# Optimization experiments

Measured on AMD Instinct MI355X. Metric: run time of the kernel, lower is better.

Reference implementation:

```python
import jax, jax.numpy as jnp
import numpy as np

VOCAB, NUM_LABELS, EMB, H = 50000, 5, 512, 1024
B, S = 32, 256


def setup_inputs() -> dict:
    key = jax.random.key(0)
    ks = jax.random.split(key, 7)
    tokens = jax.random.randint(ks[0], (B, S), 0, VOCAB)
    scale_e = 0.05
    emb = jax.random.normal(ks[1], (VOCAB, EMB), dtype=jnp.float32) * scale_e
    # Keras LSTM kernels: input kernel [EMB,4H], recurrent kernel [H,4H], bias [4H]
    W = jax.random.normal(ks[2], (EMB, 4 * H), dtype=jnp.float32) / np.sqrt(EMB)
    U = jax.random.normal(ks[3], (H, 4 * H), dtype=jnp.float32) / np.sqrt(H)
    # unit_forget_bias=True: forget-gate bias block initialized to 1
    b = jnp.concatenate([
        jnp.zeros((H,), jnp.float32),
        jnp.ones((H,), jnp.float32),
        jnp.zeros((2 * H,), jnp.float32),
    ])
    Wd = jax.random.normal(ks[4], (H, NUM_LABELS), dtype=jnp.float32) / np.sqrt(H)
    bd = jnp.zeros((NUM_LABELS,), jnp.float32)
    return {"tokens": tokens, "emb": emb, "W": W, "U": U, "b": b, "Wd": Wd, "bd": bd}


def _lstm_last_h(x, W, U, b):
    # x: [B,S,EMB] -> last hidden state [B,H]
    xt = jnp.swapaxes(x, 0, 1)  # [S,B,EMB]
    # precompute input projections for all steps: [S,B,4H]
    xz = jnp.einsum('sbe,eg->sbg', xt, W) + b
    h0 = jnp.zeros((x.shape[0], H), x.dtype)
    c0 = jnp.zeros((x.shape[0], H), x.dtype)

    def step(carry, xz_t):
        h, c = carry
        z = xz_t + h @ U  # [B,4H]
        i, f, g, o = jnp.split(z, 4, axis=-1)  # Keras gate order i,f,c,o
        i = jax.nn.sigmoid(i)
        f = jax.nn.sigmoid(f)
        g = jnp.tanh(g)
        o = jax.nn.sigmoid(o)
        c = f * c + i * g
        h = o * jnp.tanh(c)
        return (h, c), None

    (h_last, _), _ = jax.lax.scan(step, (h0, c0), xz)
    return h_last


def reference(tokens, emb, W, U, b, Wd, bd):
    x = emb[tokens]  # [B,S,EMB] embedding lookup
    h = _lstm_last_h(x, W, U, b)  # [B,H]
    logits = h @ Wd + bd  # [B,NUM_LABELS]
    return logits
```

## Files before the change

kernel.cpp:

```cpp
#include <hip/hip_runtime.h>
#include <hip/hip_fp16.h>

#define B_   32
#define S_   256
#define EMB_ 512
#define H_   1024
#define G4_  4096
#define NL_  5
#define NBLK 128

typedef short bf16x8 __attribute__((ext_vector_type(8)));
typedef _Float16 f16x8 __attribute__((ext_vector_type(8)));
typedef float f32x4 __attribute__((ext_vector_type(4)));
typedef unsigned long long ull;

__device__ inline unsigned short f2bf(float x) {
  unsigned u = __float_as_uint(x);
  return (unsigned short)((u + 0x7FFF + ((u >> 16) & 1)) >> 16);
}
__device__ inline float bf2f(unsigned short b) {
  return __uint_as_float(((unsigned)b) << 16);
}
__device__ inline ull ldq(const ull* p) {
  return __hip_atomic_load(p, __ATOMIC_RELAXED, __HIP_MEMORY_SCOPE_AGENT);
}
__device__ inline void stw(unsigned* p, unsigned v) {
  __hip_atomic_store(p, v, __ATOMIC_RELAXED, __HIP_MEMORY_SCOPE_AGENT);
}

__global__ __launch_bounds__(256) void k_transposeK(const float* __restrict__ src,
                                                    float* __restrict__ dst, int K) {
  __shared__ float tile[32][33];
  int c0 = blockIdx.x * 32, k0 = blockIdx.y * 32;
  int tx = threadIdx.x & 31, ty = threadIdx.x >> 5;
#pragma unroll
  for (int i = 0; i < 4; ++i)
    tile[ty + 8 * i][tx] = src[(size_t)(k0 + ty + 8 * i) * G4_ + c0 + tx];
  __syncthreads();
#pragma unroll
  for (int i = 0; i < 4; ++i)
    dst[(size_t)(c0 + ty + 8 * i) * K + k0 + tx] = tile[tx][ty + 8 * i];
}

__global__ __launch_bounds__(256) void k_prep(const float* __restrict__ Ut,
                                              bf16x8* __restrict__ Ubf) {
  int gid = blockIdx.x * 256 + threadIdx.x;
  int l = gid & 63;
  int bxws = gid >> 6;
  int n = l & 15, kgrp = l >> 4;
  int s = bxws & 7, bw = bxws >> 3;
  int w = bw & 3, bx = bw >> 2;
  int g = n & 3, ju = n >> 2;
  int gcol = g * 1024 + bx * 4 + ju;
  int kbase = w * 256 + s * 32 + kgrp * 8;
  const float4* f = (const float4*)(Ut + (size_t)gcol * H_ + kbase);
  float4 f0 = f[0], f1 = f[1];
  float v[8] = {f0.x, f0.y, f0.z, f0.w, f1.x, f1.y, f1.z, f1.w};
  bf16x8 vh, vl;
#pragma unroll
  for (int j = 0; j < 8; ++j) {
    unsigned short hi = f2bf(v[j]);
    vh[j] = (short)hi;
    vl[j] = (short)f2bf(v[j] - bf2f(hi));
  }
  Ubf[(size_t)bxws * 128 + l] = vh;
  Ubf[(size_t)bxws * 128 + 64 + l] = vl;
}

__global__ __launch_bounds__(256) void k_prepW16(const float* __restrict__ Wt,
                                                 unsigned short* __restrict__ Wf16) {
  int gid = blockIdx.x * 256 + threadIdx.x;
  int l = gid & 63, fi = gid >> 6;
  int kc = fi & 15, ug = fi >> 4;
  int n16 = l & 15, kgrp = l >> 4;
  int gcol = (n16 & 3) * 1024 + ug * 4 + (n16 >> 2);
  const float4* f = (const float4*)(Wt + (size_t)gcol * 512 + kc * 32 + kgrp * 8);
  float4 f0 = f[0], f1 = f[1];
  float v[8] = {f0.x, f0.y, f0.z, f0.w, f1.x, f1.y, f1.z, f1.w};
  union { unsigned short u[8]; uint4 q; } o;
#pragma unroll
  for (int j = 0; j < 8; ++j) o.u[j] = __half_as_ushort(__float2half_rn(v[j]));
  *(uint4*)(Wf16 + ((size_t)fi * 64 + l) * 8) = o.q;
}

__global__ __launch_bounds__(256) void k_prepX(const int* __restrict__ tokens,
                                               const float* __restrict__ emb,
                                               unsigned short* __restrict__ Xf16) {
  int gid = blockIdx.x * 256 + threadIdx.x;
  int seg = gid & 63, row = gid >> 6;
  int s = row >> 5, b = row & 31;
  int tok = tokens[b * 256 + s];
  const float4* f = (const float4*)(emb + (size_t)tok * EMB_ + seg * 8);
  float4 f0 = f[0], f1 = f[1];
  float v[8] = {f0.x, f0.y, f0.z, f0.w, f1.x, f1.y, f1.z, f1.w};
  union { unsigned short u[8]; uint4 q; } o;
#pragma unroll
  for (int j = 0; j < 8; ++j) o.u[j] = __half_as_ushort(__float2half_rn(v[j]));
  *(uint4*)(Xf16 + (size_t)row * 512 + seg * 8) = o.q;
}

__global__ __launch_bounds__(512, 2) void k_steps6(
    const bf16x8* __restrict__ Ubf,
    const unsigned short* __restrict__ Wf16,
    const unsigned short* __restrict__ Xf16,
    const float* __restrict__ bias,
    unsigned* __restrict__ Hh0, unsigned* __restrict__ Hl0,
    unsigned* __restrict__ Hh1, unsigned* __restrict__ Hl1,
    unsigned* __restrict__ flg) {
  __shared__ bf16x8 UL[8192];
  __shared__ float red[4096];
  __shared__ float zg[1056];
  __shared__ float bias_s[32];

  const int tid = threadIdx.x;
  const int bx = blockIdx.x;
  const int l = tid & 63, w = tid >> 6;

#pragma unroll
  for (int i = 0; i < 16; ++i) {
    int flat = i * 512 + tid;
    int ll = flat & 63, s8 = (flat >> 6) & 7, ks = (flat >> 9) & 3;
    int pl = (flat >> 11) & 1, cg = flat >> 12;
    size_t fi = (size_t)((bx * 2 + cg) * 4 + ks) * 8 + s8;
    UL[flat] = Ubf[fi * 128 + pl * 64 + ll];
  }
  if (tid < 32) {
    int cg = tid >> 4, n16 = tid & 15;
    bias_s[tid] = bias[(n16 & 3) * 1024 + (bx * 2 + cg) * 4 + (n16 >> 2)];
  }

  const int e = tid & 255, m = tid >> 8;
  const int n16r = (e >> 2) & 15;
  const int zb = m * 16 + (e >> 6) * 4 + (e & 3);

  const int gb = tid & 31, gu = tid >> 5;
  const int gk = bx * 8 + gu;
  const int widx = (gb >> 4) * 8192 + (gk >> 3) * 64 + (gb & 15) * 4 + ((gk & 7) >> 1);
  const int zrd = gb * 33 + (gu >> 2) * 16 + (gu & 3) * 4;
  float creg = 0.f;

  const int ks_w = w >> 1;
  const unsigned* myflg = flg + (w * 16 + (l & 15)) * 32;

  const int xrow0 = (l & 15) * 512 + (l >> 4) * 8;

  __syncthreads();

  for (int t = 0; t < S_; ++t) {
    const ull* RdH = (const ull*)((t & 1) ? Hh0 : Hh1);
    const ull* RdL = (const ull*)((t & 1) ? Hl0 : Hl1);
    unsigned* WrH = (t & 1) ? Hh1 : Hh0;
    unsigned* WrL = (t & 1) ? Hl1 : Hl0;

    f32x4 acc[2][2];
#pragma unroll
    for (int cg = 0; cg < 2; ++cg) {
      acc[cg][0] = (f32x4){0.f, 0.f, 0.f, 0.f};
      acc[cg][1] = (f32x4){0.f, 0.f, 0.f, 0.f};
    }
    {
      const unsigned short* Xt = Xf16 + (size_t)t * 16384;
#pragma unroll
      for (int c2 = 0; c2 < 2; ++c2) {
        int kc = w * 2 + c2;
        f16x8 xa0 = *(const f16x8*)(Xt + xrow0 + kc * 32);
        f16x8 xa1 = *(const f16x8*)(Xt + 8192 + xrow0 + kc * 32);
        f16x8 wb0 = *(const f16x8*)(Wf16 + ((size_t)((bx * 2 + 0) * 16 + kc) * 64 + l) * 8);
        f16x8 wb1 = *(const f16x8*)(Wf16 + ((size_t)((bx * 2 + 1) * 16 + kc) * 64 + l) * 8);
        acc[0][0] = __builtin_amdgcn_mfma_f32_16x16x32_f16(xa0, wb0, acc[0][0], 0, 0, 0);
        acc[0][1] = __builtin_amdgcn_mfma_f32_16x16x32_f16(xa1, wb0, acc[0][1], 0, 0, 0);
        acc[1][0] = __builtin_amdgcn_mfma_f32_16x16x32_f16(xa0, wb1, acc[1][0], 0, 0, 0);
        acc[1][1] = __builtin_amdgcn_mfma_f32_16x16x32_f16(xa1, wb1, acc[1][1], 0, 0, 0);
      }
    }

    if (t > 0) {
      while (true) {
        unsigned v = __hip_atomic_load(myflg, __ATOMIC_RELAXED, __HIP_MEMORY_SCOPE_AGENT);
        if (__all((int)(v >= (unsigned)t))) break;
        __builtin_amdgcn_s_sleep(1);
      }
      union F { ull q[2]; bf16x8 v; };
      F A[4][4];
#pragma unroll
      for (int s = 0; s < 4; ++s) {
        int i0 = (w * 16 + s * 4) * 32 + l * 2;
        A[s][0].q[0] = ldq(RdH + i0);        A[s][0].q[1] = ldq(RdH + i0 + 1);
        A[s][1].q[0] = ldq(RdH + 4096 + i0); A[s][1].q[1] = ldq(RdH + 4096 + i0 + 1);
        A[s][2].q[0] = ldq(RdL + i0);        A[s][2].q[1] = ldq(RdL + i0 + 1);
        A[s][3].q[0] = ldq(RdL + 4096 + i0); A[s][3].q[1] = ldq(RdL + 4096 + i0 + 1);
      }
#pragma unroll
      for (int s = 0; s < 4; ++s) {
        int s8 = (w & 1) * 4 + s;
#pragma unroll
        for (int cg = 0; cg < 2; ++cg) {
          bf16x8 uhf = UL[((cg * 2 + 0) * 4 + ks_w) * 512 + s8 * 64 + l];
          bf16x8 ulf = UL[((cg * 2 + 1) * 4 + ks_w) * 512 + s8 * 64 + l];
          acc[cg][0] = __builtin_amdgcn_mfma_f32_16x16x32_bf16(A[s][0].v, uhf, acc[cg][0], 0, 0, 0);
          acc[cg][1] = __builtin_amdgcn_mfma_f32_16x16x32_bf16(A[s][1].v, uhf, acc[cg][1], 0, 0, 0);
          acc[cg][0] = __builtin_amdgcn_mfma_f32_16x16x32_bf16(A[s][2].v, uhf, acc[cg][0], 0, 0, 0);
          acc[cg][1] = __builtin_amdgcn_mfma_f32_16x16x32_bf16(A[s][3].v, uhf, acc[cg][1], 0, 0, 0);
          acc[cg][0] = __builtin_amdgcn_mfma_f32_16x16x32_bf16(A[s][0].v, ulf, acc[cg][0], 0, 0, 0);
          acc[cg][1] = __builtin_amdgcn_mfma_f32_16x16x32_bf16(A[s][1].v, ulf, acc[cg][1], 0, 0, 0);
        }
      }
    }

    if (w < 4) {
#pragma unroll
      for (int cg = 0; cg < 2; ++cg) {
        *(f32x4*)(&red[((w * 2 + 0) * 2 + cg) * 256 + l * 4]) = acc[cg][0];
        *(f32x4*)(&red[((w * 2 + 1) * 2 + cg) * 256 + l * 4]) = acc[cg][1];
      }
    }
    __syncthreads();
    if (w >= 4) {
      int w4 = w - 4;
#pragma unroll
      for (int cg = 0; cg < 2; ++cg) {
        f32x4* p0 = (f32x4*)(&red[((w4 * 2 + 0) * 2 + cg) * 256 + l * 4]);
        f32x4* p1 = (f32x4*)(&red[((w4 * 2 + 1) * 2 + cg) * 256 + l * 4]);
        *p0 += acc[cg][0];
        *p1 += acc[cg][1];
      }
    }
    __syncthreads();

    {
      float z0 = bias_s[n16r], z1 = bias_s[16 + n16r];
#pragma unroll
      for (int w4 = 0; w4 < 4; ++w4) {
        z0 += red[((w4 * 2 + m) * 2 + 0) * 256 + e];
        z1 += red[((w4 * 2 + m) * 2 + 1) * 256 + e];
      }
      zg[zb * 33 + n16r] = z0;
      zg[zb * 33 + 16 + n16r] = z1;
    }
    __syncthreads();

    if (tid < 256) {
      float zi = zg[zrd + 0];
      float zf = zg[zrd + 1];
      float zc_ = zg[zrd + 2];
      float zo = zg[zrd + 3];
      float ig = 1.f / (1.f + __expf(-zi));
      float fg = 1.f / (1.f + __expf(-zf));
      float gg = tanhf(zc_);
      float og = 1.f / (1.f + __expf(-zo));
      creg = fg * creg + ig * gg;
      float hv = og * tanhf(creg);
      unsigned short hh_ = f2bf(hv);
      unsigned short hl_ = f2bf(hv - bf2f(hh_));
      unsigned pk = (unsigned)hh_ | ((unsigned)hl_ << 16);
      unsigned other = (unsigned)__shfl_xor((int)pk, 32, 64);
      if ((gu & 1) == 0)
        stw(WrH + widx, (pk & 0xffffu) | (other << 16));
      else
        stw(WrL + widx, (other >> 16) | (pk & 0xffff0000u));
    }
    __syncthreads();
    if (tid == 0)
      stw(flg + bx * 32, (unsigned)(t + 1));
  }
}

__global__ __launch_bounds__(256) void k_head4(const unsigned* __restrict__ Hh,
                                               const unsigned* __restrict__ Hl,
                                               const float* __restrict__ Wd,
                                               const float* __restrict__ bd,
                                               float* __restrict__ out) {
  __shared__ float red[32 * 9];
  int lbl = blockIdx.x;
  int tid = threadIdx.x;
  int b = tid >> 3, ks = tid & 7;
  int mb = (b >> 4) * 8192 + (b & 15) * 4;
  float acc = 0.f;
  for (int k = ks * 128; k < ks * 128 + 128; ++k) {
    int idx = mb + (k >> 3) * 64 + ((k & 7) >> 1);
    int sh = (k & 1) * 16;
    float hv = bf2f((unsigned short)((Hh[idx] >> sh) & 0xffffu)) +
               bf2f((unsigned short)((Hl[idx] >> sh) & 0xffffu));
    acc += hv * Wd[k * NL_ + lbl];
  }
  red[b * 9 + ks] = acc;
  __syncthreads();
  if (tid < 32) {
    float s = bd[lbl];
#pragma unroll
    for (int i = 0; i < 8; ++i) s += red[tid * 9 + i];
    out[tid * NL_ + lbl] = s;
  }
}

extern "C" void kernel_launch(void* const* d_in, const int* in_sizes, int n_in,
                              void* d_out, int out_size, void* d_ws, size_t ws_size,
                              hipStream_t stream) {
  const int* tokens  = (const int*)d_in[0];
  const float* emb   = (const float*)d_in[1];
  const float* W     = (const float*)d_in[2];
  const float* U     = (const float*)d_in[3];
  const float* bias  = (const float*)d_in[4];
  const float* Wd    = (const float*)d_in[5];
  const float* bd    = (const float*)d_in[6];
  float* out = (float*)d_out;

  char* ws = (char*)d_ws;
  unsigned short* Xf16 = (unsigned short*)ws;
  unsigned short* Wf16 = (unsigned short*)(ws + 8388608);
  float* Ut          = (float*)(ws + 16777216);
  float* Wt          = (float*)(ws + 33554432);
  bf16x8* Ubf        = (bf16x8*)(ws + 67108864);
  unsigned* Hh0      = (unsigned*)(ws + 83886080);
  unsigned* Hl0      = (unsigned*)(ws + 83886080 + 65536);
  unsigned* Hh1      = (unsigned*)(ws + 83886080 + 131072);
  unsigned* Hl1      = (unsigned*)(ws + 83886080 + 196608);
  unsigned* flg      = (unsigned*)(ws + 84148224);

  hipMemsetAsync(flg, 0, 16384, stream);
  k_transposeK<<<dim3(128, 32), 256, 0, stream>>>(U, Ut, 1024);
  k_prep<<<2048, 256, 0, stream>>>(Ut, Ubf);
  k_transposeK<<<dim3(128, 16), 256, 0, stream>>>(W, Wt, 512);
  k_prepW16<<<1024, 256, 0, stream>>>(Wt, Wf16);
  k_prepX<<<2048, 256, 0, stream>>>(tokens, emb, Xf16);

  k_steps6<<<NBLK, 512, 0, stream>>>(Ubf, Wf16, Xf16, bias,
                                     Hh0, Hl0, Hh1, Hl1, flg);

  k_head4<<<NL_, 256, 0, stream>>>(Hh1, Hl1, Wd, bd, out);
}
```

Baseline: 1.190 ms.

## Tag hidden-state words with step number and drop per-block flag barrier

Replaces the per-step flag counter and its trailing __syncthreads with step-tagged hidden-state words: each 32-bit store packs the fp16 h value with the step index, and readers spin on the data itself until every tag matches. The hidden state drops from a bf16 hi/lo pair to a single fp16 value, and U is split into an fp16 hi part plus a residual scaled by 1024. This cuts the recurrent MFMA count and removes one global round trip per step. In exchange, h is carried at fp16 precision, and the 16-bit step tag limits the pattern to short sequences.

```diff
diff --git a/kernel.cpp b/kernel.cpp
--- a/kernel.cpp
+++ b/kernel.cpp
@@ -9,18 +9,10 @@
 #define NL_  5
 #define NBLK 128
 
-typedef short bf16x8 __attribute__((ext_vector_type(8)));
 typedef _Float16 f16x8 __attribute__((ext_vector_type(8)));
 typedef float f32x4 __attribute__((ext_vector_type(4)));
 typedef unsigned long long ull;
 
-__device__ inline unsigned short f2bf(float x) {
-  unsigned u = __float_as_uint(x);
-  return (unsigned short)((u + 0x7FFF + ((u >> 16) & 1)) >> 16);
-}
-__device__ inline float bf2f(unsigned short b) {
-  return __uint_as_float(((unsigned)b) << 16);
-}
 __device__ inline ull ldq(const ull* p) {
   return __hip_atomic_load(p, __ATOMIC_RELAXED, __HIP_MEMORY_SCOPE_AGENT);
 }
@@ -42,8 +34,8 @@
     dst[(size_t)(c0 + ty + 8 * i) * K + k0 + tx] = tile[tx][ty + 8 * i];
 }
 
-__global__ __launch_bounds__(256) void k_prep(const float* __restrict__ Ut,
-                                              bf16x8* __restrict__ Ubf) {
+__global__ __launch_bounds__(256) void k_prepU16(const float* __restrict__ Ut,
+                                                 f16x8* __restrict__ Ubf) {
   int gid = blockIdx.x * 256 + threadIdx.x;
   int l = gid & 63;
   int bxws = gid >> 6;
@@ -56,12 +48,12 @@
   const float4* f = (const float4*)(Ut + (size_t)gcol * H_ + kbase);
   float4 f0 = f[0], f1 = f[1];
   float v[8] = {f0.x, f0.y, f0.z, f0.w, f1.x, f1.y, f1.z, f1.w};
-  bf16x8 vh, vl;
+  f16x8 vh, vl;
 #pragma unroll
   for (int j = 0; j < 8; ++j) {
-    unsigned short hi = f2bf(v[j]);
-    vh[j] = (short)hi;
-    vl[j] = (short)f2bf(v[j] - bf2f(hi));
+    _Float16 hi = (_Float16)v[j];
+    vh[j] = hi;
+    vl[j] = (_Float16)((v[j] - (float)hi) * 1024.f);
   }
   Ubf[(size_t)bxws * 128 + l] = vh;
   Ubf[(size_t)bxws * 128 + 64 + l] = vl;
@@ -99,15 +91,13 @@
   *(uint4*)(Xf16 + (size_t)row * 512 + seg * 8) = o.q;
 }
 
-__global__ __launch_bounds__(512, 2) void k_steps6(
-    const bf16x8* __restrict__ Ubf,
+__global__ __launch_bounds__(512, 2) void k_steps7(
+    const f16x8* __restrict__ Ubf,
     const unsigned short* __restrict__ Wf16,
     const unsigned short* __restrict__ Xf16,
     const float* __restrict__ bias,
-    unsigned* __restrict__ Hh0, unsigned* __restrict__ Hl0,
-    unsigned* __restrict__ Hh1, unsigned* __restrict__ Hl1,
-    unsigned* __restrict__ flg) {
-  __shared__ bf16x8 UL[8192];
+    unsigned* __restrict__ T0, unsigned* __restrict__ T1) {
+  __shared__ f16x8 UL[8192];
   __shared__ float red[4096];
   __shared__ float zg[1056];
   __shared__ float bias_s[32];
@@ -134,29 +124,27 @@
   const int zb = m * 16 + (e >> 6) * 4 + (e & 3);
 
   const int gb = tid & 31, gu = tid >> 5;
-  const int gk = bx * 8 + gu;
-  const int widx = (gb >> 4) * 8192 + (gk >> 3) * 64 + (gb & 15) * 4 + ((gk & 7) >> 1);
+  const int widx = (gb >> 4) * 16384 + (bx >> 2) * 512 +
+                   ((bx & 3) * 16 + (gb & 15)) * 8 + gu;
   const int zrd = gb * 33 + (gu >> 2) * 16 + (gu & 3) * 4;
   float creg = 0.f;
 
   const int ks_w = w >> 1;
-  const unsigned* myflg = flg + (w * 16 + (l & 15)) * 32;
-
   const int xrow0 = (l & 15) * 512 + (l >> 4) * 8;
 
   __syncthreads();
 
   for (int t = 0; t < S_; ++t) {
-    const ull* RdH = (const ull*)((t & 1) ? Hh0 : Hh1);
-    const ull* RdL = (const ull*)((t & 1) ? Hl0 : Hl1);
-    unsigned* WrH = (t & 1) ? Hh1 : Hh0;
-    unsigned* WrL = (t & 1) ? Hl1 : Hl0;
-
-    f32x4 acc[2][2];
+    const ull* R64 = (const ull*)((t & 1) ? T0 : T1);
+    unsigned* WrT = (t & 1) ? T1 : T0;
+
+    f32x4 acc[2][2], accL[2][2];
 #pragma unroll
     for (int cg = 0; cg < 2; ++cg) {
       acc[cg][0] = (f32x4){0.f, 0.f, 0.f, 0.f};
       acc[cg][1] = (f32x4){0.f, 0.f, 0.f, 0.f};
+      accL[cg][0] = (f32x4){0.f, 0.f, 0.f, 0.f};
+      accL[cg][1] = (f32x4){0.f, 0.f, 0.f, 0.f};
     }
     {
       const unsigned short* Xt = Xf16 + (size_t)t * 16384;
@@ -175,36 +163,59 @@
     }
 
     if (t > 0) {
-      while (true) {
-        unsigned v = __hip_atomic_load(myflg, __ATOMIC_RELAXED, __HIP_MEMORY_SCOPE_AGENT);
-        if (__all((int)(v >= (unsigned)t))) break;
-        __builtin_amdgcn_s_sleep(1);
-      }
-      union F { ull q[2]; bf16x8 v; };
-      F A[4][4];
-#pragma unroll
-      for (int s = 0; s < 4; ++s) {
-        int i0 = (w * 16 + s * 4) * 32 + l * 2;
-        A[s][0].q[0] = ldq(RdH + i0);        A[s][0].q[1] = ldq(RdH + i0 + 1);
-        A[s][1].q[0] = ldq(RdH + 4096 + i0); A[s][1].q[1] = ldq(RdH + 4096 + i0 + 1);
-        A[s][2].q[0] = ldq(RdL + i0);        A[s][2].q[1] = ldq(RdL + i0 + 1);
-        A[s][3].q[0] = ldq(RdL + 4096 + i0); A[s][3].q[1] = ldq(RdL + 4096 + i0 + 1);
-      }
+      ull A[2][4][4];
+      const unsigned tg = (unsigned)(t - 1);
+      bool ok;
+      do {
+#pragma unroll
+        for (int m2 = 0; m2 < 2; ++m2)
+#pragma unroll
+          for (int s = 0; s < 4; ++s) {
+            int ib = m2 * 8192 + (w * 4 + s) * 256 + l * 4;
+#pragma unroll
+            for (int i = 0; i < 4; ++i) A[m2][s][i] = ldq(R64 + ib + i);
+          }
+        unsigned bad = 0;
+#pragma unroll
+        for (int m2 = 0; m2 < 2; ++m2)
+#pragma unroll
+          for (int s = 0; s < 4; ++s)
+#pragma unroll
+            for (int i = 0; i < 4; ++i) {
+              ull q = A[m2][s][i];
+              bad |= (((unsigned)(q >> 16)) & 0xffffu) ^ tg;
+              bad |= ((unsigned)(q >> 48)) ^ tg;
+            }
+        ok = __all(bad == 0);
+        if (!ok) __builtin_amdgcn_s_sleep(1);
+      } while (!ok);
+
 #pragma unroll
       for (int s = 0; s < 4; ++s) {
         int s8 = (w & 1) * 4 + s;
+        union { unsigned u[4]; f16x8 v; } a0, a1;
+#pragma unroll
+        for (int i = 0; i < 4; ++i) {
+          ull q0 = A[0][s][i], q1 = A[1][s][i];
+          a0.u[i] = ((unsigned)q0 & 0xffffu) | (((unsigned)(q0 >> 16)) & 0xffff0000u);
+          a1.u[i] = ((unsigned)q1 & 0xffffu) | (((unsigned)(q1 >> 16)) & 0xffff0000u);
+        }
 #pragma unroll
         for (int cg = 0; cg < 2; ++cg) {
-          bf16x8 uhf = UL[((cg * 2 + 0) * 4 + ks_w) * 512 + s8 * 64 + l];
-          bf16x8 ulf = UL[((cg * 2 + 1) * 4 + ks_w) * 512 + s8 * 64 + l];
-          acc[cg][0] = __builtin_amdgcn_mfma_f32_16x16x32_bf16(A[s][0].v, uhf, acc[cg][0], 0, 0, 0);
-          acc[cg][1] = __builtin_amdgcn_mfma_f32_16x16x32_bf16(A[s][1].v, uhf, acc[cg][1], 0, 0, 0);
-          acc[cg][0] = __builtin_amdgcn_mfma_f32_16x16x32_bf16(A[s][2].v, uhf, acc[cg][0], 0, 0, 0);
-          acc[cg][1] = __builtin_amdgcn_mfma_f32_16x16x32_bf16(A[s][3].v, uhf, acc[cg][1], 0, 0, 0);
-          acc[cg][0] = __builtin_amdgcn_mfma_f32_16x16x32_bf16(A[s][0].v, ulf, acc[cg][0], 0, 0, 0);
-          acc[cg][1] = __builtin_amdgcn_mfma_f32_16x16x32_bf16(A[s][1].v, ulf, acc[cg][1], 0, 0, 0);
+          f16x8 uhf = UL[cg * 4096 + ks_w * 512 + s8 * 64 + l];
+          f16x8 ulf = UL[cg * 4096 + 2048 + ks_w * 512 + s8 * 64 + l];
+          acc[cg][0]  = __builtin_amdgcn_mfma_f32_16x16x32_f16(a0.v, uhf, acc[cg][0], 0, 0, 0);
+          acc[cg][1]  = __builtin_amdgcn_mfma_f32_16x16x32_f16(a1.v, uhf, acc[cg][1], 0, 0, 0);
+          accL[cg][0] = __builtin_amdgcn_mfma_f32_16x16x32_f16(a0.v, ulf, accL[cg][0], 0, 0, 0);
+          accL[cg][1] = __builtin_amdgcn_mfma_f32_16x16x32_f16(a1.v, ulf, accL[cg][1], 0, 0, 0);
         }
       }
+    }
+
+#pragma unroll
+    for (int cg = 0; cg < 2; ++cg) {
+      acc[cg][0] += accL[cg][0] * 9.765625e-4f;
+      acc[cg][1] += accL[cg][1] * 9.765625e-4f;
     }
 
     if (w < 4) {
@@ -250,23 +261,13 @@
       float og = 1.f / (1.f + __expf(-zo));
       creg = fg * creg + ig * gg;
       float hv = og * tanhf(creg);
-      unsigned short hh_ = f2bf(hv);
-      unsigned short hl_ = f2bf(hv - bf2f(hh_));
-      unsigned pk = (unsigned)hh_ | ((unsigned)hl_ << 16);
-      unsigned other = (unsigned)__shfl_xor((int)pk, 32, 64);
-      if ((gu & 1) == 0)
-        stw(WrH + widx, (pk & 0xffffu) | (other << 16));
-      else
-        stw(WrL + widx, (other >> 16) | (pk & 0xffff0000u));
-    }
-    __syncthreads();
-    if (tid == 0)
-      stw(flg + bx * 32, (unsigned)(t + 1));
-  }
-}
-
-__global__ __launch_bounds__(256) void k_head4(const unsigned* __restrict__ Hh,
-                                               const unsigned* __restrict__ Hl,
+      unsigned short h16 = __half_as_ushort(__float2half_rn(hv));
+      stw(WrT + widx, ((unsigned)t << 16) | (unsigned)h16);
+    }
+  }
+}
+
+__global__ __launch_bounds__(256) void k_head5(const unsigned* __restrict__ T,
                                                const float* __restrict__ Wd,
                                                const float* __restrict__ bd,
                                                float* __restrict__ out) {
@@ -274,13 +275,11 @@
   int lbl = blockIdx.x;
   int tid = threadIdx.x;
   int b = tid >> 3, ks = tid & 7;
-  int mb = (b >> 4) * 8192 + (b & 15) * 4;
+  int mb = (b >> 4) * 16384;
   float acc = 0.f;
   for (int k = ks * 128; k < ks * 128 + 128; ++k) {
-    int idx = mb + (k >> 3) * 64 + ((k & 7) >> 1);
-    int sh = (k & 1) * 16;
-    float hv = bf2f((unsigned short)((Hh[idx] >> sh) & 0xffffu)) +
-               bf2f((unsigned short)((Hl[idx] >> sh) & 0xffffu));
+    int idx = mb + (k >> 5) * 512 + (((k >> 3) & 3) * 16 + (b & 15)) * 8 + (k & 7);
+    float hv = __half2float(__ushort_as_half((unsigned short)(T[idx] & 0xffffu)));
     acc += hv * Wd[k * NL_ + lbl];
   }
   red[b * 9 + ks] = acc;
@@ -310,22 +309,18 @@
   unsigned short* Wf16 = (unsigned short*)(ws + 8388608);
   float* Ut          = (float*)(ws + 16777216);
   float* Wt          = (float*)(ws + 33554432);
-  bf16x8* Ubf        = (bf16x8*)(ws + 67108864);
-  unsigned* Hh0      = (unsigned*)(ws + 83886080);
-  unsigned* Hl0      = (unsigned*)(ws + 83886080 + 65536);
-  unsigned* Hh1      = (unsigned*)(ws + 83886080 + 131072);
-  unsigned* Hl1      = (unsigned*)(ws + 83886080 + 196608);
-  unsigned* flg      = (unsigned*)(ws + 84148224);
-
-  hipMemsetAsync(flg, 0, 16384, stream);
+  f16x8* Ubf         = (f16x8*)(ws + 67108864);
+  unsigned* T0       = (unsigned*)(ws + 83886080);
+  unsigned* T1       = (unsigned*)(ws + 83886080 + 131072);
+
+  hipMemsetAsync(T0, 0xFF, 262144, stream);
   k_transposeK<<<dim3(128, 32), 256, 0, stream>>>(U, Ut, 1024);
-  k_prep<<<2048, 256, 0, stream>>>(Ut, Ubf);
+  k_prepU16<<<2048, 256, 0, stream>>>(Ut, Ubf);
   k_transposeK<<<dim3(128, 16), 256, 0, stream>>>(W, Wt, 512);
   k_prepW16<<<1024, 256, 0, stream>>>(Wt, Wf16);
   k_prepX<<<2048, 256, 0, stream>>>(tokens, emb, Xf16);
 
-  k_steps6<<<NBLK, 512, 0, stream>>>(Ubf, Wf16, Xf16, bias,
-                                     Hh0, Hl0, Hh1, Hl1, flg);
-
-  k_head4<<<NL_, 256, 0, stream>>>(Hh1, Hl1, Wd, bd, out);
-}
+  k_steps7<<<NBLK, 512, 0, stream>>>(Ubf, Wf16, Xf16, bias, T0, T1);
+
+  k_head5<<<NL_, 256, 0, stream>>>(T1, Wd, bd, out);
+}
```

New measurement: 1.714 ms. 44.0% more time.
